# Kernel optimization log

Hardware: AMD Instinct MI355X
Metric: run time of the kernel (lower is better)

The kernel has to match this reference:

```python
import jax, jax.numpy as jnp
import numpy as np

B, N, CIN, H, OUT, E = 64, 512, 128, 256, 12, 8192


def setup_inputs() -> dict:
    key = jax.random.key(0)
    ks = jax.random.split(key, 32)
    g = lambda i, shape, s=0.05: jax.random.normal(ks[i], shape, jnp.float32) * s
    inp = {
        "x": jax.random.normal(ks[0], (B, N, CIN), jnp.float32),
        "edge_index": jax.random.randint(ks[1], (2, E), 0, N),
        "edge_weight": jax.random.uniform(ks[2], (E,), dtype=jnp.float32),
    }
    # TGCN2 gate params: GCNConv lin (CIN->H, bias added after aggregation) + Linear(2H->H)
    for j, gate in enumerate(["z", "r", "h"]):
        base = 3 + j * 4
        inp[f"W{gate}"] = g(base, (CIN, H))
        inp[f"b{gate}"] = jnp.zeros((H,), jnp.float32)
        inp[f"l{gate}_W"] = g(base + 1, (2 * H, H))
        inp[f"l{gate}_b"] = jnp.zeros((H,), jnp.float32)
    # 2-layer GRU (torch layout: W_ih [3H,in], W_hh [3H,H]); eval mode (dropout off)
    inp["Wih0"] = g(16, (3 * H, CIN)); inp["Whh0"] = g(17, (3 * H, H))
    inp["bih0"] = jnp.zeros((3 * H,), jnp.float32); inp["bhh0"] = jnp.zeros((3 * H,), jnp.float32)
    inp["Wih1"] = g(18, (3 * H, H)); inp["Whh1"] = g(19, (3 * H, H))
    inp["bih1"] = jnp.zeros((3 * H,), jnp.float32); inp["bhh1"] = jnp.zeros((3 * H,), jnp.float32)
    # heads (stored as [in,out] so y = x @ W + b, matching torch x @ W.T + b)
    inp["l1_W"] = g(20, (H, 1)); inp["l1_b"] = jnp.zeros((1,), jnp.float32)
    inp["l2_W"] = g(21, (H, 1)); inp["l2_b"] = jnp.zeros((1,), jnp.float32)
    inp["l3_W"] = g(22, (2, OUT)); inp["l3_b"] = jnp.zeros((OUT,), jnp.float32)
    return inp


def _gcn_norm(edge_index, edge_weight, n_nodes):
    # improved=True -> self loops with fill value 2.0; sym normalization
    loop = jnp.arange(n_nodes)
    src = jnp.concatenate([edge_index[0], loop])
    tgt = jnp.concatenate([edge_index[1], loop])
    ew = jnp.concatenate([edge_weight, jnp.full((n_nodes,), 2.0, edge_weight.dtype)])
    deg = jax.ops.segment_sum(ew, tgt, num_segments=n_nodes)
    dinv = jnp.where(deg > 0, deg ** -0.5, 0.0)
    return src, tgt, dinv[src] * ew * dinv[tgt]


def _gcn_conv(x, W, b, src, tgt, norm):
    xw = x @ W                                   # [B,N,H]
    msg = xw[:, src, :] * norm[None, :, None]    # gather from sources [B,E+N,H]
    out = jnp.zeros_like(xw).at[:, tgt, :].add(msg)  # scatter-add to targets
    return out + b


def _gru_layer(x_sbf, Wih, Whh, bih, bhh):
    h_dim = Whh.shape[1]
    h0 = jnp.zeros((x_sbf.shape[1], h_dim), x_sbf.dtype)

    def step(h, xt):
        gi = xt @ Wih.T + bih
        gh = h @ Whh.T + bhh
        ir, iz, inn = jnp.split(gi, 3, axis=-1)
        hr, hz, hn = jnp.split(gh, 3, axis=-1)
        r = jax.nn.sigmoid(ir + hr)
        z = jax.nn.sigmoid(iz + hz)
        n = jnp.tanh(inn + r * hn)
        h_new = (1.0 - z) * n + z * h
        return h_new, h_new

    _, ys = jax.lax.scan(step, h0, x_sbf)
    return ys  # [S,B,H]


def reference(x, edge_index, edge_weight, Wz, bz, lz_W, lz_b, Wr, br, lr_W, lr_b,
              Wh, bh, lh_W, lh_b, Wih0, Whh0, bih0, bhh0, Wih1, Whh1, bih1, bhh1,
              l1_W, l1_b, l2_W, l2_b, l3_W, l3_b):
    n_nodes = x.shape[1]
    # GRU branch (node dim treated as sequence, as in the source)
    xs = jnp.transpose(x, (1, 0, 2))             # [N,B,CIN]
    h1 = _gru_layer(xs, Wih0, Whh0, bih0, bhh0)
    h2 = _gru_layer(h1, Wih1, Whh1, bih1, bhh1)
    temp = jnp.transpose(h2, (1, 0, 2))          # [B,N,H]
    gru_out = temp @ l2_W + l2_b                 # [B,N,1]
    # TGCN2 cell with H0 = 0
    src, tgt, norm = _gcn_norm(edge_index, edge_weight, n_nodes)
    Hst = jnp.zeros((x.shape[0], n_nodes, lz_W.shape[1]), x.dtype)
    cz = _gcn_conv(x, Wz, bz, src, tgt, norm)
    Z = jax.nn.sigmoid(jnp.concatenate([cz, Hst], axis=2) @ lz_W + lz_b)
    cr = _gcn_conv(x, Wr, br, src, tgt, norm)
    R = jax.nn.sigmoid(jnp.concatenate([cr, Hst], axis=2) @ lr_W + lr_b)
    ch = _gcn_conv(x, Wh, bh, src, tgt, norm)
    H_tilde = jnp.tanh(jnp.concatenate([ch, Hst * R], axis=2) @ lh_W + lh_b)
    Hn = Z * Hst + (1.0 - Z) * H_tilde           # [B,N,H]
    h = jax.nn.relu(Hn) @ l1_W + l1_b            # [B,N,1]
    cat = jnp.concatenate([gru_out, h], axis=2)  # [B,N,2]
    return cat @ l3_W + l3_b                     # [B,N,OUT]
```

## Files before the change

### kernel.cpp

```cpp
#include <hip/hip_runtime.h>


typedef unsigned short u16;
typedef unsigned long long u64;
typedef short s8v __attribute__((ext_vector_type(8)));
typedef float f4v __attribute__((ext_vector_type(4)));

#define NBATCH 64
#define NNODE  512
#define DCIN   128
#define DHID   256
#define NEDGE  8192
#define RING   8
#define SLOTU16 16384

__device__ __forceinline__ u16 f2b(float f) {
    union { float f; unsigned int i; } v; v.f = f;
    unsigned int x = v.i;
    return (u16)((x + 0x7FFFu + ((x >> 16) & 1u)) >> 16);
}
__device__ __forceinline__ float sigm(float x)  { return 1.0f / (1.0f + __expf(-x)); }
__device__ __forceinline__ float tanh_(float x) { return 1.0f - 2.0f / (1.0f + __expf(2.0f * x)); }
__device__ __forceinline__ f4v mfma16(s8v a, s8v b, f4v c) {
    return __builtin_amdgcn_mfma_f32_16x16x32_bf16(a, b, c, 0, 0, 0);
}
__device__ __forceinline__ s8v ld_ring(const u64* p) {
    union { u64 d[2]; s8v v; } u;
    u.d[0] = __hip_atomic_load(p,     __ATOMIC_RELAXED, __HIP_MEMORY_SCOPE_AGENT);
    u.d[1] = __hip_atomic_load(p + 1, __ATOMIC_RELAXED, __HIP_MEMORY_SCOPE_AGENT);
    return u.v;
}
__device__ __forceinline__ void st_ring(u64* p, s8v v) {
    union { s8v v; u64 d[2]; } u; u.v = v;
    __hip_atomic_store(p,     u.d[0], __ATOMIC_RELAXED, __HIP_MEMORY_SCOPE_AGENT);
    __hip_atomic_store(p + 1, u.d[1], __ATOMIC_RELAXED, __HIP_MEMORY_SCOPE_AGENT);
}

__global__ void init_kernel(float* deg, int* counts, int* flags) {
    int i = blockIdx.x * blockDim.x + threadIdx.x;
    if (i < NNODE) { deg[i] = 2.0f; counts[i] = 1; }
    if (i < 128) flags[i] = 0;
}

__global__ void edge_deg_kernel(const int* __restrict__ ei, const float* __restrict__ ew,
                                float* deg, int* counts) {
    int e = blockIdx.x * blockDim.x + threadIdx.x;
    if (e < NEDGE) {
        int t = ei[NEDGE + e];
        atomicAdd(&deg[t], ew[e]);
        atomicAdd(&counts[t], 1);
    }
}

__global__ void scan_kernel(const float* __restrict__ deg, const int* __restrict__ counts,
                            float* __restrict__ dinv, int* __restrict__ rowptr,
                            int* __restrict__ cursor, int* __restrict__ col,
                            float* __restrict__ val) {
    __shared__ int sc[NNODE];
    int i = threadIdx.x;
    float d = deg[i];
    float di = (d > 0.0f) ? (1.0f / sqrtf(d)) : 0.0f;
    dinv[i] = di;
    int cnt = counts[i];
    sc[i] = cnt;
    __syncthreads();
    for (int ofs = 1; ofs < NNODE; ofs <<= 1) {
        int add = (i >= ofs) ? sc[i - ofs] : 0;
        __syncthreads();
        sc[i] += add;
        __syncthreads();
    }
    int ex = sc[i] - cnt;
    rowptr[i] = ex;
    if (i == NNODE - 1) rowptr[NNODE] = sc[NNODE - 1];
    col[ex] = i;
    val[ex] = di * 2.0f * di;
    cursor[i] = ex + 1;
}

__global__ void fill_kernel(const int* __restrict__ ei, const float* __restrict__ ew,
                            const float* __restrict__ dinv, int* cursor,
                            int* __restrict__ col, float* __restrict__ val) {
    int e = blockIdx.x * blockDim.x + threadIdx.x;
    if (e < NEDGE) {
        int s = ei[e], t = ei[NEDGE + e];
        int p = atomicAdd(&cursor[t], 1);
        col[p] = s;
        val[p] = dinv[s] * ew[e] * dinv[t];
    }
}

__global__ void fold_kernel(const float* __restrict__ Wz, const float* __restrict__ lzW,
                            const float* __restrict__ bz, const float* __restrict__ lzb,
                            const float* __restrict__ Wh, const float* __restrict__ lhW,
                            const float* __restrict__ bh, const float* __restrict__ lhb,
                            u16* __restrict__ Wf, float* __restrict__ bfold) {
    int nidx = blockIdx.x;
    int g = nidx & 1, j = nidx >> 1;
    int k = threadIdx.x;
    const float* W = g ? Wh : Wz;
    const float* L = g ? lhW : lzW;
    float acc = 0.0f;
    for (int m = 0; m < DHID; ++m)
        acc += W[k * DHID + m] * L[m * DHID + j];
    Wf[nidx * DCIN + k] = f2b(acc);
    if (k == 0) {
        const float* bg = g ? bh : bz;
        const float* lb = g ? lhb : lzb;
        float ab = 0.0f;
        for (int m = 0; m < DHID; ++m) ab += bg[m] * L[m * DHID + j];
        bfold[nidx] = ab + lb[j];
    }
}

__global__ void repack_w_kernel(const float* __restrict__ Wih, const float* __restrict__ Whh,
                                int KCX, int KC, int KX, int KH, u16* __restrict__ dst) {
    int id = blockIdx.x * 256 + threadIdx.x;
    int total = 16 * KC * 3 * 64;
    if (id >= total) return;
    int l = id & 63; int rest = id >> 6;
    int g = rest % 3; rest /= 3;
    int kc = rest % KC; rest /= KC;
    int r = rest;
    int j = r * 16 + (l & 15);
    int q = l >> 4;
    const float* src; int k;
    if (kc < KCX) { src = Wih + (size_t)(g * 256 + j) * KX; k = kc * 32 + q * 8; }
    else          { src = Whh + (size_t)(g * 256 + j) * KH; k = (kc - KCX) * 32 + q * 8; }
    u16* d = dst + (((size_t)(r * KC + kc)) * 3 + g) * 512 + l * 8;
    #pragma unroll
    for (int e = 0; e < 8; ++e) d[e] = f2b(src[k + e]);
}

__global__ void repack_x_kernel(const float* __restrict__ x, u16* __restrict__ xpack) {
    int id = blockIdx.x * 256 + threadIdx.x;
    int l = id & 63; int rest = id >> 6;
    int kc = rest & 3; rest >>= 2;
    int Mt = rest & 3; rest >>= 2;
    int t = rest;
    int b = Mt * 16 + (l & 15);
    int c = kc * 32 + (l >> 4) * 8;
    const float* s = x + ((size_t)b * NNODE + t) * DCIN + c;
    u16* d = xpack + (((size_t)t * 4 + Mt) * 4 + kc) * 512 + (size_t)l * 8;
    #pragma unroll
    for (int e = 0; e < 8; ++e) d[e] = f2b(s[e]);
}

__global__ __launch_bounds__(256)
void tgcn_kernel(const float* __restrict__ x, const int* __restrict__ rowptr,
                 const int* __restrict__ col, const float* __restrict__ val,
                 const u16* __restrict__ Wf, const float* __restrict__ bfold,
                 const float* __restrict__ l1W, float* __restrict__ hdot) {
    __shared__ u16 As[64][136];
    const int tid = threadIdx.x;
    const int bx = blockIdx.x;
    const int b = bx >> 3;
    const int n0 = (bx & 7) * 64;
    {
        const int c = tid & 127;
        const int half = tid >> 7;
        for (int it = 0; it < 32; ++it) {
            int r = it * 2 + half;
            int n = n0 + r;
            int s = rowptr[n], e = rowptr[n + 1];
            float acc = 0.0f;
            for (int i = s; i < e; ++i)
                acc += val[i] * x[((size_t)b * NNODE + col[i]) * DCIN + c];
            As[r][c] = f2b(acc);
        }
    }
    __syncthreads();
    const int w = tid >> 6, l = tid & 63;
    const int ncol = l & 15, q = l >> 4, ko = q * 8;
    s8v af[4];
    #pragma unroll
    for (int kc = 0; kc < 4; ++kc)
        af[kc] = *(const s8v*)(&As[w * 16 + ncol][kc * 32 + ko]);
    float partial[4] = {0.f, 0.f, 0.f, 0.f};
    for (int nc = 0; nc < 32; ++nc) {
        int n = nc * 16 + ncol;
        const u16* brow = Wf + (size_t)n * DCIN + ko;
        f4v acc = {0.f, 0.f, 0.f, 0.f};
        #pragma unroll
        for (int kc = 0; kc < 4; ++kc)
            acc = mfma16(af[kc], *(const s8v*)(brow + kc * 32), acc);
        float bias = bfold[n];
        float l1w = l1W[n >> 1];
        #pragma unroll
        for (int rr = 0; rr < 4; ++rr) {
            float v = acc[rr] + bias;
            float o = __shfl_xor(v, 1);
            float zpre = (ncol & 1) ? o : v;
            float hpre = (ncol & 1) ? v : o;
            float hn = (1.0f - sigm(zpre)) * tanh_(hpre);
            hn = hn > 0.0f ? hn : 0.0f;
            if (!(ncol & 1)) partial[rr] += hn * l1w;
        }
    }
    #pragma unroll
    for (int rr = 0; rr < 4; ++rr) {
        float p = partial[rr];
        p += __shfl_xor(p, 1); p += __shfl_xor(p, 2);
        p += __shfl_xor(p, 4); p += __shfl_xor(p, 8);
        if (ncol == 0)
            hdot[bx * 64 + w * 16 + q * 4 + rr] = p;
    }
}

__global__ __launch_bounds__(256)
void gru_pipe_kernel(const u16* __restrict__ xpack,
                     const u16* __restrict__ Wpk0, const u16* __restrict__ Wpk1,
                     const float* __restrict__ bih0, const float* __restrict__ bhh0,
                     const float* __restrict__ bih1, const float* __restrict__ bhh1,
                     const float* __restrict__ l2W,
                     u16* __restrict__ h0ring, u16* __restrict__ h1ring,
                     int* flags, float* __restrict__ gpartg) {
    __shared__ u16 wlds[16 * 3 * 512];
    __shared__ u16 tile[4][16][16];

    const int tid = threadIdx.x;
    const int w = tid >> 6;
    const int l = tid & 63;
    const int q = l >> 4, ncol = l & 15;
    const bool isL1 = blockIdx.x >= 16;
    const int rblk = blockIdx.x & 15;
    const int KC = isL1 ? 16 : 12;

    int* fL0 = flags;
    int* fL1 = flags + 16;

    {
        const s8v* src = (const s8v*)((isL1 ? Wpk1 : Wpk0) + (size_t)rblk * KC * 3 * 512);
        s8v* dst = (s8v*)wlds;
        for (int i = tid; i < KC * 3 * 64; i += 256) dst[i] = src[i];
    }
    const int j = rblk * 16 + ncol;
    const float* bihp = isL1 ? bih1 : bih0;
    const float* bhhp = isL1 ? bhh1 : bhh0;
    const float br = bihp[j] + bhhp[j];
    const float bz = bihp[256 + j] + bhhp[256 + j];
    const float bi = bihp[512 + j];
    const float bhn = bhhp[512 + j];
    const float l2v = isL1 ? l2W[j] : 0.0f;
    float hreg[4] = {0.f, 0.f, 0.f, 0.f};
    const int qbase = 2 * (rblk & 1);
    u16* myring = isL1 ? h1ring : h0ring;
    const s8v* wf = (const s8v*)wlds;
    __syncthreads();

    for (int t = 0; t < NNODE; ++t) {
        {
            int tgt0 = isL1 ? t + 1 : t;
            int tgt1 = isL1 ? t : t - 7;
            while (true) {
                int v, tg;
                if (l < 16)      { v = __hip_atomic_load(fL0 + l, __ATOMIC_RELAXED, __HIP_MEMORY_SCOPE_AGENT); tg = tgt0; }
                else if (l < 32) { v = __hip_atomic_load(fL1 + (l - 16), __ATOMIC_RELAXED, __HIP_MEMORY_SCOPE_AGENT); tg = tgt1; }
                else             { v = 0; tg = -0x7fffffff; }
                if (__all(v >= tg)) break;
                __builtin_amdgcn_s_sleep(2);
            }
            asm volatile("" ::: "memory");
        }
        s8v a0[8], a1[8];
        if (isL1) {
            const u64* s0 = (const u64*)(h0ring + (size_t)(t & (RING - 1)) * SLOTU16);
            #pragma unroll
            for (int k = 0; k < 8; ++k) a0[k] = ld_ring(s0 + (size_t)(w * 8 + k) * 128 + l * 2);
            if (t > 0) {
                const u64* s1 = (const u64*)(h1ring + (size_t)((t - 1) & (RING - 1)) * SLOTU16);
                #pragma unroll
                for (int k = 0; k < 8; ++k) a1[k] = ld_ring(s1 + (size_t)(w * 8 + k) * 128 + l * 2);
            }
        } else {
            #pragma unroll
            for (int k = 0; k < 4; ++k)
                a0[k] = *(const s8v*)(xpack + (((size_t)t * 4 + w) * 4 + k) * 512 + (size_t)l * 8);
            if (t > 0) {
                const u64* s1 = (const u64*)(h0ring + (size_t)((t - 1) & (RING - 1)) * SLOTU16);
                #pragma unroll
                for (int k = 0; k < 8; ++k) a1[k] = ld_ring(s1 + (size_t)(w * 8 + k) * 128 + l * 2);
            }
        }
        f4v accR = {0,0,0,0}, accZ = {0,0,0,0}, accNi = {0,0,0,0}, accNh = {0,0,0,0};
        if (isL1) {
            #pragma unroll
            for (int kc = 0; kc < 8; ++kc) {
                accR  = mfma16(a0[kc], wf[(kc * 3 + 0) * 64 + l], accR);
                accZ  = mfma16(a0[kc], wf[(kc * 3 + 1) * 64 + l], accZ);
                accNi = mfma16(a0[kc], wf[(kc * 3 + 2) * 64 + l], accNi);
            }
            if (t > 0) {
                #pragma unroll
                for (int k = 0; k < 8; ++k) {
                    int kc = 8 + k;
                    accR  = mfma16(a1[k], wf[(kc * 3 + 0) * 64 + l], accR);
                    accZ  = mfma16(a1[k], wf[(kc * 3 + 1) * 64 + l], accZ);
                    accNh = mfma16(a1[k], wf[(kc * 3 + 2) * 64 + l], accNh);
                }
            }
        } else {
            #pragma unroll
            for (int kc = 0; kc < 4; ++kc) {
                accR  = mfma16(a0[kc], wf[(kc * 3 + 0) * 64 + l], accR);
                accZ  = mfma16(a0[kc], wf[(kc * 3 + 1) * 64 + l], accZ);
                accNi = mfma16(a0[kc], wf[(kc * 3 + 2) * 64 + l], accNi);
            }
            if (t > 0) {
                #pragma unroll
                for (int k = 0; k < 8; ++k) {
                    int kc = 4 + k;
                    accR  = mfma16(a1[k], wf[(kc * 3 + 0) * 64 + l], accR);
                    accZ  = mfma16(a1[k], wf[(kc * 3 + 1) * 64 + l], accZ);
                    accNh = mfma16(a1[k], wf[(kc * 3 + 2) * 64 + l], accNh);
                }
            }
        }
        float pd[4];
        #pragma unroll
        for (int rr = 0; rr < 4; ++rr) {
            float rv = sigm(accR[rr] + br);
            float zv = sigm(accZ[rr] + bz);
            float nv = tanh_(accNi[rr] + bi + rv * (accNh[rr] + bhn));
            float hn = nv + zv * (hreg[rr] - nv);
            hreg[rr] = hn;
            tile[w][q * 4 + rr][ncol] = f2b(hn);
            pd[rr] = hn * l2v;
        }
        if (isL1) {
            #pragma unroll
            for (int rr = 0; rr < 4; ++rr) {
                float v = pd[rr];
                v += __shfl_xor(v, 1); v += __shfl_xor(v, 2);
                v += __shfl_xor(v, 4); v += __shfl_xor(v, 8);
                if (ncol == 0)
                    gpartg[((size_t)t * 16 + rblk) * 64 + w * 16 + q * 4 + rr] = v;
            }
        }
        if (q == qbase || q == qbase + 1) {
            s8v v = *(const s8v*)&tile[w][ncol][8 * (q - qbase)];
            u64* dst = (u64*)(myring + (size_t)(t & (RING - 1)) * SLOTU16)
                       + (size_t)(w * 8 + (rblk >> 1)) * 128 + l * 2;
            st_ring(dst, v);
        }
        __syncthreads();
        if (tid == 0)
            __hip_atomic_store((isL1 ? fL1 : fL0) + rblk, t + 1,
                               __ATOMIC_RELAXED, __HIP_MEMORY_SCOPE_AGENT);
    }
}

__global__ __launch_bounds__(256)
void head_kernel(const float* __restrict__ gpartg, const float* __restrict__ hdot,
                 const float* __restrict__ l1b, const float* __restrict__ l2b,
                 const float* __restrict__ l3W, const float* __restrict__ l3b,
                 float* __restrict__ out) {
    int idx = blockIdx.x * 256 + threadIdx.x;
    if (idx >= NBATCH * NNODE * 12) return;
    int r = idx / 12, oc = idx - r * 12;
    int b = r >> 9, n = r & 511;
    float g = 0.0f;
    #pragma unroll
    for (int k = 0; k < 16; ++k) g += gpartg[((size_t)n * 16 + k) * 64 + b];
    g += l2b[0];
    float hh = hdot[r] + l1b[0];
    out[idx] = g * l3W[oc] + hh * l3W[12 + oc] + l3b[oc];
}

static hipStream_t g_side = nullptr;
static hipEvent_t  g_evA  = nullptr;
static hipEvent_t  g_evB  = nullptr;
namespace {
struct SideInit {
    SideInit() {
        if (hipStreamCreateWithFlags(&g_side, hipStreamNonBlocking) != hipSuccess) g_side = nullptr;
        if (hipEventCreateWithFlags(&g_evA, hipEventDisableTiming) != hipSuccess) g_evA = nullptr;
        if (hipEventCreateWithFlags(&g_evB, hipEventDisableTiming) != hipSuccess) g_evB = nullptr;
    }
};
static SideInit g_side_init;
}

extern "C" void kernel_launch(void* const* d_in, const int* in_sizes, int n_in,
                              void* d_out, int out_size, void* d_ws, size_t ws_size,
                              hipStream_t stream) {
    const float* x    = (const float*)d_in[0];
    const int*   ei   = (const int*)  d_in[1];
    const float* ew   = (const float*)d_in[2];
    const float* Wz   = (const float*)d_in[3];
    const float* bz   = (const float*)d_in[4];
    const float* lzW  = (const float*)d_in[5];
    const float* lzb  = (const float*)d_in[6];
    const float* Wh   = (const float*)d_in[11];
    const float* bh   = (const float*)d_in[12];
    const float* lhW  = (const float*)d_in[13];
    const float* lhb  = (const float*)d_in[14];
    const float* Wih0 = (const float*)d_in[15];
    const float* Whh0 = (const float*)d_in[16];
    const float* bih0 = (const float*)d_in[17];
    const float* bhh0 = (const float*)d_in[18];
    const float* Wih1 = (const float*)d_in[19];
    const float* Whh1 = (const float*)d_in[20];
    const float* bih1 = (const float*)d_in[21];
    const float* bhh1 = (const float*)d_in[22];
    const float* l1W  = (const float*)d_in[23];
    const float* l1b  = (const float*)d_in[24];
    const float* l2W  = (const float*)d_in[25];
    const float* l2b  = (const float*)d_in[26];
    const float* l3W  = (const float*)d_in[27];
    const float* l3b  = (const float*)d_in[28];

    char* ws = (char*)d_ws;
    size_t o = 0;
    auto take = [&](size_t nbytes) {
        char* p = ws + o;
        o = (o + nbytes + 255) & ~(size_t)255;
        return p;
    };
    float* deg    = (float*)take(NNODE * 4);
    float* dinv   = (float*)take(NNODE * 4);
    int*   rowptr = (int*)  take((NNODE + 1) * 4);
    int*   cursor = (int*)  take(NNODE * 4);
    int*   col    = (int*)  take((NEDGE + NNODE) * 4);
    float* val    = (float*)take((NEDGE + NNODE) * 4);
    u16*   Wf     = (u16*)  take((size_t)512 * DCIN * 2);
    float* bfold  = (float*)take(512 * 4);
    float* hdot   = (float*)take((size_t)NBATCH * NNODE * 4);
    float* gpartg = (float*)take((size_t)NNODE * 16 * 64 * 4);
    u16*   xpack  = (u16*)  take((size_t)NNODE * 4 * 4 * 512 * 2);
    u16*   Wpk0   = (u16*)  take((size_t)16 * 12 * 3 * 512 * 2);
    u16*   Wpk1   = (u16*)  take((size_t)16 * 16 * 3 * 512 * 2);
    u16*   h0ring = (u16*)  take((size_t)RING * SLOTU16 * 2);
    u16*   h1ring = (u16*)  take((size_t)RING * SLOTU16 * 2);
    int*   flags  = (int*)  take(512);
    if (o > ws_size) return;

    const bool fork = (g_side && g_evA && g_evB);
    hipStream_t sideS = fork ? g_side : stream;

    init_kernel<<<2, 256, 0, stream>>>(deg, cursor, flags);

    if (fork) {
        hipEventRecord(g_evA, stream);
        hipStreamWaitEvent(sideS, g_evA, 0);
    }

    edge_deg_kernel<<<NEDGE / 256, 256, 0, sideS>>>(ei, ew, deg, cursor);
    scan_kernel<<<1, NNODE, 0, sideS>>>(deg, cursor, dinv, rowptr, cursor, col, val);
    fill_kernel<<<NEDGE / 256, 256, 0, sideS>>>(ei, ew, dinv, cursor, col, val);
    fold_kernel<<<512, DCIN, 0, sideS>>>(Wz, lzW, bz, lzb, Wh, lhW, bh, lhb, Wf, bfold);
    tgcn_kernel<<<512, 256, 0, sideS>>>(x, rowptr, col, val, Wf, bfold, l1W, hdot);
    if (fork) hipEventRecord(g_evB, sideS);

    repack_w_kernel<<<(16 * 12 * 3 * 64 + 255) / 256, 256, 0, stream>>>(
        Wih0, Whh0, 4, 12, DCIN, DHID, Wpk0);
    repack_w_kernel<<<(16 * 16 * 3 * 64 + 255) / 256, 256, 0, stream>>>(
        Wih1, Whh1, 8, 16, DHID, DHID, Wpk1);
    repack_x_kernel<<<(NNODE * 4 * 4 * 64) / 256, 256, 0, stream>>>(x, xpack);
    gru_pipe_kernel<<<32, 256, 0, stream>>>(xpack, Wpk0, Wpk1, bih0, bhh0,
                                            bih1, bhh1, l2W, h0ring, h1ring,
                                            flags, gpartg);

    if (fork) hipStreamWaitEvent(stream, g_evB, 0);
    head_kernel<<<(NBATCH * NNODE * 12 + 255) / 256, 256, 0, stream>>>(
        gpartg, hdot, l1b, l2b, l3W, l3b, (float*)d_out);
    (void)in_sizes; (void)n_in; (void)out_size;
}
```

Baseline: 2.777 ms.

## Halve GRU pipeline block count by giving each block two column chunks

The persistent GRU pipeline kernel is templated on the number of blocks per layer. By default it runs 8 blocks per layer, each owning 32 hidden columns, with 96KB of dynamic LDS for the weights, instead of 16 blocks of 16 columns. Fewer blocks mean fewer flags to poll and less cross-block synchronization on each of the 512 sequential steps. In exchange each block does twice the MFMA work per step, which lengthens the serial critical path per step.

```diff
diff --git a/kernel.cpp b/kernel.cpp
--- a/kernel.cpp
+++ b/kernel.cpp
@@ -207,6 +207,7 @@
     }
 }
 
+template <int NBLK>
 __global__ __launch_bounds__(256)
 void gru_pipe_kernel(const u16* __restrict__ xpack,
                      const u16* __restrict__ Wpk0, const u16* __restrict__ Wpk1,
@@ -215,37 +216,48 @@
                      const float* __restrict__ l2W,
                      u16* __restrict__ h0ring, u16* __restrict__ h1ring,
                      int* flags, float* __restrict__ gpartg) {
-    __shared__ u16 wlds[16 * 3 * 512];
-    __shared__ u16 tile[4][16][16];
+    constexpr int CPB = 256 / NBLK;
+    constexpr int NCI = CPB / 16;
+    extern __shared__ u16 wlds_dyn[];
+    __shared__ u16 tile[4][16][CPB];
 
     const int tid = threadIdx.x;
     const int w = tid >> 6;
     const int l = tid & 63;
     const int q = l >> 4, ncol = l & 15;
-    const bool isL1 = blockIdx.x >= 16;
-    const int rblk = blockIdx.x & 15;
+    const bool isL1 = blockIdx.x >= NBLK;
+    const int rblk = isL1 ? (blockIdx.x - NBLK) : blockIdx.x;
     const int KC = isL1 ? 16 : 12;
 
     int* fL0 = flags;
     int* fL1 = flags + 16;
 
     {
-        const s8v* src = (const s8v*)((isL1 ? Wpk1 : Wpk0) + (size_t)rblk * KC * 3 * 512);
-        s8v* dst = (s8v*)wlds;
-        for (int i = tid; i < KC * 3 * 64; i += 256) dst[i] = src[i];
-    }
-    const int j = rblk * 16 + ncol;
+        const s8v* src = (const s8v*)((isL1 ? Wpk1 : Wpk0)
+                                      + (size_t)rblk * NCI * (KC * 3 * 512));
+        s8v* dst = (s8v*)wlds_dyn;
+        for (int i = tid; i < NCI * KC * 3 * 64; i += 256) dst[i] = src[i];
+    }
     const float* bihp = isL1 ? bih1 : bih0;
     const float* bhhp = isL1 ? bhh1 : bhh0;
-    const float br = bihp[j] + bhhp[j];
-    const float bz = bihp[256 + j] + bhhp[256 + j];
-    const float bi = bihp[512 + j];
-    const float bhn = bhhp[512 + j];
-    const float l2v = isL1 ? l2W[j] : 0.0f;
-    float hreg[4] = {0.f, 0.f, 0.f, 0.f};
+    float br[NCI], bz[NCI], bi[NCI], bhn[NCI], l2v[NCI];
+    #pragma unroll
+    for (int ci = 0; ci < NCI; ++ci) {
+        int j = rblk * CPB + ci * 16 + ncol;
+        br[ci]  = bihp[j] + bhhp[j];
+        bz[ci]  = bihp[256 + j] + bhhp[256 + j];
+        bi[ci]  = bihp[512 + j];
+        bhn[ci] = bhhp[512 + j];
+        l2v[ci] = isL1 ? l2W[j] : 0.0f;
+    }
+    float hreg[NCI][4];
+    #pragma unroll
+    for (int ci = 0; ci < NCI; ++ci)
+        #pragma unroll
+        for (int rr = 0; rr < 4; ++rr) hreg[ci][rr] = 0.0f;
     const int qbase = 2 * (rblk & 1);
     u16* myring = isL1 ? h1ring : h0ring;
-    const s8v* wf = (const s8v*)wlds;
+    const s8v* wf = (const s8v*)wlds_dyn;
     __syncthreads();
 
     for (int t = 0; t < NNODE; ++t) {
@@ -253,10 +265,9 @@
             int tgt0 = isL1 ? t + 1 : t;
             int tgt1 = isL1 ? t : t - 7;
             while (true) {
-                int v, tg;
-                if (l < 16)      { v = __hip_atomic_load(fL0 + l, __ATOMIC_RELAXED, __HIP_MEMORY_SCOPE_AGENT); tg = tgt0; }
-                else if (l < 32) { v = __hip_atomic_load(fL1 + (l - 16), __ATOMIC_RELAXED, __HIP_MEMORY_SCOPE_AGENT); tg = tgt1; }
-                else             { v = 0; tg = -0x7fffffff; }
+                int v = 0x7fffffff, tg = -0x7fffffff;
+                if (l < NBLK)                      { v = __hip_atomic_load(fL0 + l, __ATOMIC_RELAXED, __HIP_MEMORY_SCOPE_AGENT); tg = tgt0; }
+                else if (l >= 16 && l < 16 + NBLK) { v = __hip_atomic_load(fL1 + (l - 16), __ATOMIC_RELAXED, __HIP_MEMORY_SCOPE_AGENT); tg = tgt1; }
                 if (__all(v >= tg)) break;
                 __builtin_amdgcn_s_sleep(2);
             }
@@ -282,50 +293,66 @@
                 for (int k = 0; k < 8; ++k) a1[k] = ld_ring(s1 + (size_t)(w * 8 + k) * 128 + l * 2);
             }
         }
-        f4v accR = {0,0,0,0}, accZ = {0,0,0,0}, accNi = {0,0,0,0}, accNh = {0,0,0,0};
+        f4v accR[NCI], accZ[NCI], accNi[NCI], accNh[NCI];
+        #pragma unroll
+        for (int ci = 0; ci < NCI; ++ci) {
+            accR[ci] = f4v{0,0,0,0}; accZ[ci] = f4v{0,0,0,0};
+            accNi[ci] = f4v{0,0,0,0}; accNh[ci] = f4v{0,0,0,0};
+        }
         if (isL1) {
             #pragma unroll
-            for (int kc = 0; kc < 8; ++kc) {
-                accR  = mfma16(a0[kc], wf[(kc * 3 + 0) * 64 + l], accR);
-                accZ  = mfma16(a0[kc], wf[(kc * 3 + 1) * 64 + l], accZ);
-                accNi = mfma16(a0[kc], wf[(kc * 3 + 2) * 64 + l], accNi);
-            }
-            if (t > 0) {
+            for (int ci = 0; ci < NCI; ++ci) {
+                const s8v* wfc = wf + ci * (16 * 3 * 64);
                 #pragma unroll
-                for (int k = 0; k < 8; ++k) {
-                    int kc = 8 + k;
-                    accR  = mfma16(a1[k], wf[(kc * 3 + 0) * 64 + l], accR);
-                    accZ  = mfma16(a1[k], wf[(kc * 3 + 1) * 64 + l], accZ);
-                    accNh = mfma16(a1[k], wf[(kc * 3 + 2) * 64 + l], accNh);
+                for (int kc = 0; kc < 8; ++kc) {
+                    accR[ci]  = mfma16(a0[kc], wfc[(kc * 3 + 0) * 64 + l], accR[ci]);
+                    accZ[ci]  = mfma16(a0[kc], wfc[(kc * 3 + 1) * 64 + l], accZ[ci]);
+                    accNi[ci] = mfma16(a0[kc], wfc[(kc * 3 + 2) * 64 + l], accNi[ci]);
+                }
+                if (t > 0) {
+                    #pragma unroll
+                    for (int k = 0; k < 8; ++k) {
+                        int kc = 8 + k;
+                        accR[ci]  = mfma16(a1[k], wfc[(kc * 3 + 0) * 64 + l], accR[ci]);
+                        accZ[ci]  = mfma16(a1[k], wfc[(kc * 3 + 1) * 64 + l], accZ[ci]);
+                        accNh[ci] = mfma16(a1[k], wfc[(kc * 3 + 2) * 64 + l], accNh[ci]);
+                    }
                 }
             }
         } else {
             #pragma unroll
-            for (int kc = 0; kc < 4; ++kc) {
-                accR  = mfma16(a0[kc], wf[(kc * 3 + 0) * 64 + l], accR);
-                accZ  = mfma16(a0[kc], wf[(kc * 3 + 1) * 64 + l], accZ);
-                accNi = mfma16(a0[kc], wf[(kc * 3 + 2) * 64 + l], accNi);
-            }
-            if (t > 0) {
+            for (int ci = 0; ci < NCI; ++ci) {
+                const s8v* wfc = wf + ci * (12 * 3 * 64);
                 #pragma unroll
-                for (int k = 0; k < 8; ++k) {
-                    int kc = 4 + k;
-                    accR  = mfma16(a1[k], wf[(kc * 3 + 0) * 64 + l], accR);
-                    accZ  = mfma16(a1[k], wf[(kc * 3 + 1) * 64 + l], accZ);
-                    accNh = mfma16(a1[k], wf[(kc * 3 + 2) * 64 + l], accNh);
+                for (int kc = 0; kc < 4; ++kc) {
+                    accR[ci]  = mfma16(a0[kc], wfc[(kc * 3 + 0) * 64 + l], accR[ci]);
+                    accZ[ci]  = mfma16(a0[kc], wfc[(kc * 3 + 1) * 64 + l], accZ[ci]);
+                    accNi[ci] = mfma16(a0[kc], wfc[(kc * 3 + 2) * 64 + l], accNi[ci]);
                 }
-            }
-        }
-        float pd[4];
+                if (t > 0) {
+                    #pragma unroll
+                    for (int k = 0; k < 8; ++k) {
+                        int kc = 4 + k;
+                        accR[ci]  = mfma16(a1[k], wfc[(kc * 3 + 0) * 64 + l], accR[ci]);
+                        accZ[ci]  = mfma16(a1[k], wfc[(kc * 3 + 1) * 64 + l], accZ[ci]);
+                        accNh[ci] = mfma16(a1[k], wfc[(kc * 3 + 2) * 64 + l], accNh[ci]);
+                    }
+                }
+            }
+        }
+        float pd[4] = {0.f, 0.f, 0.f, 0.f};
         #pragma unroll
-        for (int rr = 0; rr < 4; ++rr) {
-            float rv = sigm(accR[rr] + br);
-            float zv = sigm(accZ[rr] + bz);
-            float nv = tanh_(accNi[rr] + bi + rv * (accNh[rr] + bhn));
-            float hn = nv + zv * (hreg[rr] - nv);
-            hreg[rr] = hn;
-            tile[w][q * 4 + rr][ncol] = f2b(hn);
-            pd[rr] = hn * l2v;
+        for (int ci = 0; ci < NCI; ++ci) {
+            #pragma unroll
+            for (int rr = 0; rr < 4; ++rr) {
+                float rv = sigm(accR[ci][rr] + br[ci]);
+                float zv = sigm(accZ[ci][rr] + bz[ci]);
+                float nv = tanh_(accNi[ci][rr] + bi[ci] + rv * (accNh[ci][rr] + bhn[ci]));
+                float hn = nv + zv * (hreg[ci][rr] - nv);
+                hreg[ci][rr] = hn;
+                tile[w][q * 4 + rr][ci * 16 + ncol] = f2b(hn);
+                pd[rr] += hn * l2v[ci];
+            }
         }
         if (isL1) {
             #pragma unroll
@@ -334,14 +361,18 @@
                 v += __shfl_xor(v, 1); v += __shfl_xor(v, 2);
                 v += __shfl_xor(v, 4); v += __shfl_xor(v, 8);
                 if (ncol == 0)
-                    gpartg[((size_t)t * 16 + rblk) * 64 + w * 16 + q * 4 + rr] = v;
-            }
-        }
-        if (q == qbase || q == qbase + 1) {
-            s8v v = *(const s8v*)&tile[w][ncol][8 * (q - qbase)];
-            u64* dst = (u64*)(myring + (size_t)(t & (RING - 1)) * SLOTU16)
-                       + (size_t)(w * 8 + (rblk >> 1)) * 128 + l * 2;
-            st_ring(dst, v);
+                    gpartg[((size_t)t * NBLK + rblk) * 64 + w * 16 + q * 4 + rr] = v;
+            }
+        }
+        u64* slot = (u64*)(myring + (size_t)(t & (RING - 1)) * SLOTU16);
+        if (NCI == 2) {
+            s8v v = *(const s8v*)&tile[w][l & 15][(l >> 4) * 8];
+            st_ring(slot + (size_t)(w * 8 + rblk) * 128 + l * 2, v);
+        } else {
+            if (q == qbase || q == qbase + 1) {
+                s8v v = *(const s8v*)&tile[w][ncol][8 * (q - qbase)];
+                st_ring(slot + (size_t)(w * 8 + (rblk >> 1)) * 128 + l * 2, v);
+            }
         }
         __syncthreads();
         if (tid == 0)
@@ -354,14 +385,13 @@
 void head_kernel(const float* __restrict__ gpartg, const float* __restrict__ hdot,
                  const float* __restrict__ l1b, const float* __restrict__ l2b,
                  const float* __restrict__ l3W, const float* __restrict__ l3b,
-                 float* __restrict__ out) {
+                 float* __restrict__ out, int nblk) {
     int idx = blockIdx.x * 256 + threadIdx.x;
     if (idx >= NBATCH * NNODE * 12) return;
     int r = idx / 12, oc = idx - r * 12;
     int b = r >> 9, n = r & 511;
     float g = 0.0f;
-    #pragma unroll
-    for (int k = 0; k < 16; ++k) g += gpartg[((size_t)n * 16 + k) * 64 + b];
+    for (int k = 0; k < nblk; ++k) g += gpartg[((size_t)n * nblk + k) * 64 + b];
     g += l2b[0];
     float hh = hdot[r] + l1b[0];
     out[idx] = g * l3W[oc] + hh * l3W[12 + oc] + l3b[oc];
@@ -370,12 +400,16 @@
 static hipStream_t g_side = nullptr;
 static hipEvent_t  g_evA  = nullptr;
 static hipEvent_t  g_evB  = nullptr;
+static bool        g_dyn96_ok = false;
 namespace {
 struct SideInit {
     SideInit() {
         if (hipStreamCreateWithFlags(&g_side, hipStreamNonBlocking) != hipSuccess) g_side = nullptr;
         if (hipEventCreateWithFlags(&g_evA, hipEventDisableTiming) != hipSuccess) g_evA = nullptr;
         if (hipEventCreateWithFlags(&g_evB, hipEventDisableTiming) != hipSuccess) g_evB = nullptr;
+        g_dyn96_ok = (hipFuncSetAttribute((const void*)&gru_pipe_kernel<8>,
+                                          hipFuncAttributeMaxDynamicSharedMemorySize,
+                                          96 * 1024) == hipSuccess);
     }
 };
 static SideInit g_side_init;
@@ -457,12 +491,22 @@
     repack_w_kernel<<<(16 * 16 * 3 * 64 + 255) / 256, 256, 0, stream>>>(
         Wih1, Whh1, 8, 16, DHID, DHID, Wpk1);
     repack_x_kernel<<<(NNODE * 4 * 4 * 64) / 256, 256, 0, stream>>>(x, xpack);
-    gru_pipe_kernel<<<32, 256, 0, stream>>>(xpack, Wpk0, Wpk1, bih0, bhh0,
-                                            bih1, bhh1, l2W, h0ring, h1ring,
-                                            flags, gpartg);
+
+    int nblk;
+    if (g_dyn96_ok) {
+        nblk = 8;
+        gru_pipe_kernel<8><<<16, 256, 96 * 1024, stream>>>(
+            xpack, Wpk0, Wpk1, bih0, bhh0, bih1, bhh1, l2W,
+            h0ring, h1ring, flags, gpartg);
+    } else {
+        nblk = 16;
+        gru_pipe_kernel<16><<<32, 256, 48 * 1024, stream>>>(
+            xpack, Wpk0, Wpk1, bih0, bhh0, bih1, bhh1, l2W,
+            h0ring, h1ring, flags, gpartg);
+    }
 
     if (fork) hipStreamWaitEvent(stream, g_evB, 0);
     head_kernel<<<(NBATCH * NNODE * 12 + 255) / 256, 256, 0, stream>>>(
-        gpartg, hdot, l1b, l2b, l3W, l3b, (float*)d_out);
+        gpartg, hdot, l1b, l2b, l3W, l3b, (float*)d_out, nblk);
     (void)in_sizes; (void)n_in; (void)out_size;
 }
```

After: 2.786 ms. No clear change (+0.3%).

## Split GRU flag waits to overlap independent MFMAs and fuse x conversion

Applied to the files above, without the earlier changes.

Layer 0 now computes its input-projection MFMAs straight from fp32 x, converting to bf16 inline, before waiting on the ring flags. Layer 1 waits separately for its own previous state and for layer 0's output, so the recurrent MFMAs can run while layer 0 is still producing. This removes the repack_x kernel and its buffer and takes independent work off the serial critical path of the 512-step recurrence. In exchange, layer 0 issues uncoalesced fp32 loads of x on every step.

```diff
diff --git a/kernel.cpp b/kernel.cpp
--- a/kernel.cpp
+++ b/kernel.cpp
@@ -34,6 +34,32 @@
     union { s8v v; u64 d[2]; } u; u.v = v;
     __hip_atomic_store(p,     u.d[0], __ATOMIC_RELAXED, __HIP_MEMORY_SCOPE_AGENT);
     __hip_atomic_store(p + 1, u.d[1], __ATOMIC_RELAXED, __HIP_MEMORY_SCOPE_AGENT);
+}
+__device__ __forceinline__ void wait_joint(const int* f, int tgtf,
+                                           const int* g, int tgtg, int l) {
+    while (true) {
+        int v = 0x7fffffff, tg = -0x7fffffff;
+        if (l < 16)      { v = __hip_atomic_load(f + l, __ATOMIC_RELAXED, __HIP_MEMORY_SCOPE_AGENT); tg = tgtf; }
+        else if (l < 32) { v = __hip_atomic_load(g + (l - 16), __ATOMIC_RELAXED, __HIP_MEMORY_SCOPE_AGENT); tg = tgtg; }
+        if (__all(v >= tg)) break;
+        __builtin_amdgcn_s_sleep(2);
+    }
+    asm volatile("" ::: "memory");
+}
+__device__ __forceinline__ void wait_one(const int* f, int tgt, int l) {
+    while (true) {
+        int v = 0x7fffffff;
+        if (l < 16) v = __hip_atomic_load(f + l, __ATOMIC_RELAXED, __HIP_MEMORY_SCOPE_AGENT);
+        if (__all(v >= tgt)) break;
+        __builtin_amdgcn_s_sleep(2);
+    }
+    asm volatile("" ::: "memory");
+}
+__device__ __forceinline__ s8v cvt8(const float* p) {
+    s8v r;
+    #pragma unroll
+    for (int e = 0; e < 8; ++e) r[e] = (short)f2b(p[e]);
+    return r;
 }
 
 __global__ void init_kernel(float* deg, int* counts, int* flags) {
@@ -130,20 +156,6 @@
     u16* d = dst + (((size_t)(r * KC + kc)) * 3 + g) * 512 + l * 8;
     #pragma unroll
     for (int e = 0; e < 8; ++e) d[e] = f2b(src[k + e]);
-}
-
-__global__ void repack_x_kernel(const float* __restrict__ x, u16* __restrict__ xpack) {
-    int id = blockIdx.x * 256 + threadIdx.x;
-    int l = id & 63; int rest = id >> 6;
-    int kc = rest & 3; rest >>= 2;
-    int Mt = rest & 3; rest >>= 2;
-    int t = rest;
-    int b = Mt * 16 + (l & 15);
-    int c = kc * 32 + (l >> 4) * 8;
-    const float* s = x + ((size_t)b * NNODE + t) * DCIN + c;
-    u16* d = xpack + (((size_t)t * 4 + Mt) * 4 + kc) * 512 + (size_t)l * 8;
-    #pragma unroll
-    for (int e = 0; e < 8; ++e) d[e] = f2b(s[e]);
 }
 
 __global__ __launch_bounds__(256)
@@ -208,7 +220,7 @@
 }
 
 __global__ __launch_bounds__(256)
-void gru_pipe_kernel(const u16* __restrict__ xpack,
+void gru_pipe_kernel(const float* __restrict__ x,
                      const u16* __restrict__ Wpk0, const u16* __restrict__ Wpk1,
                      const float* __restrict__ bih0, const float* __restrict__ bhh0,
                      const float* __restrict__ bih1, const float* __restrict__ bhh1,
@@ -246,51 +258,43 @@
     const int qbase = 2 * (rblk & 1);
     u16* myring = isL1 ? h1ring : h0ring;
     const s8v* wf = (const s8v*)wlds;
+    const float* xrow = x + ((size_t)(w * 16 + ncol) * NNODE) * DCIN + q * 8;
     __syncthreads();
 
     for (int t = 0; t < NNODE; ++t) {
-        {
-            int tgt0 = isL1 ? t + 1 : t;
-            int tgt1 = isL1 ? t : t - 7;
-            while (true) {
-                int v, tg;
-                if (l < 16)      { v = __hip_atomic_load(fL0 + l, __ATOMIC_RELAXED, __HIP_MEMORY_SCOPE_AGENT); tg = tgt0; }
-                else if (l < 32) { v = __hip_atomic_load(fL1 + (l - 16), __ATOMIC_RELAXED, __HIP_MEMORY_SCOPE_AGENT); tg = tgt1; }
-                else             { v = 0; tg = -0x7fffffff; }
-                if (__all(v >= tg)) break;
-                __builtin_amdgcn_s_sleep(2);
+        f4v accR = {0,0,0,0}, accZ = {0,0,0,0}, accNi = {0,0,0,0}, accNh = {0,0,0,0};
+        if (!isL1) {
+            const float* xp = xrow + (size_t)t * DCIN;
+            #pragma unroll
+            for (int kc = 0; kc < 4; ++kc) {
+                s8v a = cvt8(xp + kc * 32);
+                accR  = mfma16(a, wf[(kc * 3 + 0) * 64 + l], accR);
+                accZ  = mfma16(a, wf[(kc * 3 + 1) * 64 + l], accZ);
+                accNi = mfma16(a, wf[(kc * 3 + 2) * 64 + l], accNi);
             }
-            asm volatile("" ::: "memory");
-        }
-        s8v a0[8], a1[8];
-        if (isL1) {
-            const u64* s0 = (const u64*)(h0ring + (size_t)(t & (RING - 1)) * SLOTU16);
-            #pragma unroll
-            for (int k = 0; k < 8; ++k) a0[k] = ld_ring(s0 + (size_t)(w * 8 + k) * 128 + l * 2);
+            wait_joint(fL0, t, fL1, t - 7, l);
             if (t > 0) {
-                const u64* s1 = (const u64*)(h1ring + (size_t)((t - 1) & (RING - 1)) * SLOTU16);
+                const u64* s1 = (const u64*)(h0ring + (size_t)((t - 1) & (RING - 1)) * SLOTU16);
+                s8v a1[8];
                 #pragma unroll
-                for (int k = 0; k < 8; ++k) a1[k] = ld_ring(s1 + (size_t)(w * 8 + k) * 128 + l * 2);
+                for (int k = 0; k < 8; ++k)
+                    a1[k] = ld_ring(s1 + (size_t)(w * 8 + k) * 128 + l * 2);
+                #pragma unroll
+                for (int k = 0; k < 8; ++k) {
+                    int kc = 4 + k;
+                    accR  = mfma16(a1[k], wf[(kc * 3 + 0) * 64 + l], accR);
+                    accZ  = mfma16(a1[k], wf[(kc * 3 + 1) * 64 + l], accZ);
+                    accNh = mfma16(a1[k], wf[(kc * 3 + 2) * 64 + l], accNh);
+                }
             }
         } else {
-            #pragma unroll
-            for (int k = 0; k < 4; ++k)
-                a0[k] = *(const s8v*)(xpack + (((size_t)t * 4 + w) * 4 + k) * 512 + (size_t)l * 8);
             if (t > 0) {
-                const u64* s1 = (const u64*)(h0ring + (size_t)((t - 1) & (RING - 1)) * SLOTU16);
+                wait_one(fL1, t, l);
+                const u64* s1 = (const u64*)(h1ring + (size_t)((t - 1) & (RING - 1)) * SLOTU16);
+                s8v a1[8];
                 #pragma unroll
-                for (int k = 0; k < 8; ++k) a1[k] = ld_ring(s1 + (size_t)(w * 8 + k) * 128 + l * 2);
-            }
-        }
-        f4v accR = {0,0,0,0}, accZ = {0,0,0,0}, accNi = {0,0,0,0}, accNh = {0,0,0,0};
-        if (isL1) {
-            #pragma unroll
-            for (int kc = 0; kc < 8; ++kc) {
-                accR  = mfma16(a0[kc], wf[(kc * 3 + 0) * 64 + l], accR);
-                accZ  = mfma16(a0[kc], wf[(kc * 3 + 1) * 64 + l], accZ);
-                accNi = mfma16(a0[kc], wf[(kc * 3 + 2) * 64 + l], accNi);
-            }
-            if (t > 0) {
+                for (int k = 0; k < 8; ++k)
+                    a1[k] = ld_ring(s1 + (size_t)(w * 8 + k) * 128 + l * 2);
                 #pragma unroll
                 for (int k = 0; k < 8; ++k) {
                     int kc = 8 + k;
@@ -299,21 +303,17 @@
                     accNh = mfma16(a1[k], wf[(kc * 3 + 2) * 64 + l], accNh);
                 }
             }
-        } else {
+            wait_one(fL0, t + 1, l);
+            const u64* s0 = (const u64*)(h0ring + (size_t)(t & (RING - 1)) * SLOTU16);
+            s8v a0[8];
             #pragma unroll
-            for (int kc = 0; kc < 4; ++kc) {
-                accR  = mfma16(a0[kc], wf[(kc * 3 + 0) * 64 + l], accR);
-                accZ  = mfma16(a0[kc], wf[(kc * 3 + 1) * 64 + l], accZ);
-                accNi = mfma16(a0[kc], wf[(kc * 3 + 2) * 64 + l], accNi);
-            }
-            if (t > 0) {
-                #pragma unroll
-                for (int k = 0; k < 8; ++k) {
-                    int kc = 4 + k;
-                    accR  = mfma16(a1[k], wf[(kc * 3 + 0) * 64 + l], accR);
-                    accZ  = mfma16(a1[k], wf[(kc * 3 + 1) * 64 + l], accZ);
-                    accNh = mfma16(a1[k], wf[(kc * 3 + 2) * 64 + l], accNh);
-                }
+            for (int k = 0; k < 8; ++k)
+                a0[k] = ld_ring(s0 + (size_t)(w * 8 + k) * 128 + l * 2);
+            #pragma unroll
+            for (int k = 0; k < 8; ++k) {
+                accR  = mfma16(a0[k], wf[(k * 3 + 0) * 64 + l], accR);
+                accZ  = mfma16(a0[k], wf[(k * 3 + 1) * 64 + l], accZ);
+                accNi = mfma16(a0[k], wf[(k * 3 + 2) * 64 + l], accNi);
             }
         }
         float pd[4];
@@ -427,7 +427,6 @@
     float* bfold  = (float*)take(512 * 4);
     float* hdot   = (float*)take((size_t)NBATCH * NNODE * 4);
     float* gpartg = (float*)take((size_t)NNODE * 16 * 64 * 4);
-    u16*   xpack  = (u16*)  take((size_t)NNODE * 4 * 4 * 512 * 2);
     u16*   Wpk0   = (u16*)  take((size_t)16 * 12 * 3 * 512 * 2);
     u16*   Wpk1   = (u16*)  take((size_t)16 * 16 * 3 * 512 * 2);
     u16*   h0ring = (u16*)  take((size_t)RING * SLOTU16 * 2);
@@ -456,8 +455,7 @@
         Wih0, Whh0, 4, 12, DCIN, DHID, Wpk0);
     repack_w_kernel<<<(16 * 16 * 3 * 64 + 255) / 256, 256, 0, stream>>>(
         Wih1, Whh1, 8, 16, DHID, DHID, Wpk1);
-    repack_x_kernel<<<(NNODE * 4 * 4 * 64) / 256, 256, 0, stream>>>(x, xpack);
-    gru_pipe_kernel<<<32, 256, 0, stream>>>(xpack, Wpk0, Wpk1, bih0, bhh0,
+    gru_pipe_kernel<<<32, 256, 0, stream>>>(x, Wpk0, Wpk1, bih0, bhh0,
                                             bih1, bhh1, l2W, h0ring, h1ring,
                                             flags, gpartg);
 
```

Result: faster. 2.374 ms (-14.5%).
